# Kernel tuning notes

Hardware: AMD Instinct MI355X
Metric: run time of the kernel (lower is better)

The kernel has to match this reference:

```python
import jax, jax.numpy as jnp
import numpy as np

B, S, D = 2, 2048, 2048
H, KVH = 16, 8
HD = D // H          # 128
REP = H // KVH       # 2
FF = 5504
EPS = 1e-5
THETA = 1e6


def rotate_half(x):
    h = x.shape[-1] // 2
    return jnp.concatenate([-x[..., h:], x[..., :h]], axis=-1)


def rms_norm(x, g):
    v = jnp.mean(x.astype(jnp.float32) ** 2, axis=-1, keepdims=True)
    return (x * jax.lax.rsqrt(v + EPS)).astype(x.dtype) * g


def setup_inputs() -> dict:
    key = jax.random.key(0)
    ks = jax.random.split(key, 10)
    # RoPE tables [S, HD]
    inv_freq = 1.0 / (THETA ** (np.arange(0, HD, 2, dtype=np.float32) / HD))
    t = np.arange(S, dtype=np.float32)
    freqs = np.outer(t, inv_freq)                      # [S, HD/2]
    emb = np.concatenate([freqs, freqs], axis=-1)      # [S, HD]
    sc = 0.02
    return {
        "x": jax.random.normal(ks[0], (B, S, D), jnp.float32),
        "cos": jnp.asarray(np.cos(emb)),
        "sin": jnp.asarray(np.sin(emb)),
        "wq": jax.random.normal(ks[1], (H * HD, D), jnp.float32) * sc,
        "wk": jax.random.normal(ks[2], (KVH * HD, D), jnp.float32) * sc,
        "wv": jax.random.normal(ks[3], (KVH * HD, D), jnp.float32) * sc,
        "wo": jax.random.normal(ks[4], (D, H * HD), jnp.float32) * sc,
        "w_gate": jax.random.normal(ks[5], (FF, D), jnp.float32) * sc,
        "w_up": jax.random.normal(ks[6], (FF, D), jnp.float32) * sc,
        "w_down": jax.random.normal(ks[7], (D, FF), jnp.float32) * sc,
        "g1": jnp.ones((D,), jnp.float32),
        "g2": jnp.ones((D,), jnp.float32),
    }


def reference(x, cos, sin, wq, wk, wv, wo, w_gate, w_up, w_down, g1, g2):
    # ---- attention sub-block ----
    h = rms_norm(x, g1)
    q = (h @ wq.T).reshape(B, S, H, HD)
    k = (h @ wk.T).reshape(B, S, KVH, HD)
    v = (h @ wv.T).reshape(B, S, KVH, HD)
    # RoPE: cos/sin [S,HD] -> broadcast over (B, S, heads, HD) via unsqueeze at head dim
    c = cos[:S][:, None, :]
    s = sin[:S][:, None, :]
    q = q * c + rotate_half(q) * s
    k = k * c + rotate_half(k) * s
    # GQA repeat_kv (repeat_interleave on head dim), then bshd -> bhsd
    k = jnp.repeat(k, REP, axis=2).transpose(0, 2, 1, 3)
    v = jnp.repeat(v, REP, axis=2).transpose(0, 2, 1, 3)
    q = q.transpose(0, 2, 1, 3)
    scores = jnp.einsum("bhqd,bhkd->bhqk", q, k) / jnp.sqrt(jnp.float32(HD))
    causal = jnp.triu(jnp.full((S, S), -jnp.inf, jnp.float32), k=1)
    scores = scores + causal[None, None]
    attn = jax.nn.softmax(scores.astype(jnp.float32), axis=-1).astype(scores.dtype)
    out = jnp.einsum("bhqk,bhkd->bhqd", attn, v)
    out = out.transpose(0, 2, 1, 3).reshape(B, S, H * HD)
    x = x + out @ wo.T
    # ---- SwiGLU MLP sub-block ----
    h2 = rms_norm(x, g2)
    mlp = (jax.nn.silu(h2 @ w_gate.T) * (h2 @ w_up.T)) @ w_down.T
    return x + mlp
```

## Files before the change

kernel.cpp:

```cpp
#include <hip/hip_runtime.h>

#define DM 2048
#define SEQ 2048
#define HD 128
#define FF_ 5504
#define QK_SCALE_L2E 0.12751744f

typedef __bf16 bf16x8 __attribute__((ext_vector_type(8)));
typedef float f32x4 __attribute__((ext_vector_type(4)));
typedef float f32x16 __attribute__((ext_vector_type(16)));
typedef unsigned short u16x8 __attribute__((ext_vector_type(8)));
typedef unsigned int u32x4 __attribute__((ext_vector_type(4)));

typedef __attribute__((address_space(1))) void* gas1;
typedef __attribute__((address_space(3))) void* las3;
#define GLDS16(g, s) __builtin_amdgcn_global_load_lds((gas1)(g), (las3)(s), 16, 0, 0)

static __device__ __forceinline__ float bf2f(unsigned short u) {
  union { unsigned int i; float f; } c; c.i = ((unsigned int)u) << 16; return c.f;
}
static __device__ __forceinline__ unsigned short f2bf(float f) {
  __bf16 b = (__bf16)f;
  return __builtin_bit_cast(unsigned short, b);
}
static __device__ __forceinline__ unsigned int pk2(float a, float b) {
  return (unsigned int)f2bf(a) | ((unsigned int)f2bf(b) << 16);
}
static __device__ __forceinline__ float fexp2(float x) { return exp2f(x); }

__global__ __launch_bounds__(256) void k_convW(const float* __restrict__ wq,
                                               const float* __restrict__ wk,
                                               const float* __restrict__ wv,
                                               const float* __restrict__ wo,
                                               unsigned short* __restrict__ wqkv,
                                               unsigned short* __restrict__ wo_bf) {
  int b = blockIdx.x;
  const float* src;
  unsigned short* dst;
  if (b < 2048)      { src = wq + (size_t)b * DM;            dst = wqkv + (size_t)b * DM; }
  else if (b < 3072) { src = wk + (size_t)(b - 2048) * DM;   dst = wqkv + 4194304 + (size_t)(b - 2048) * DM; }
  else if (b < 4096) { src = wv + (size_t)(b - 3072) * DM;   dst = wqkv + 6291456 + (size_t)(b - 3072) * DM; }
  else               { src = wo + (size_t)(b - 4096) * DM;   dst = wo_bf + (size_t)(b - 4096) * DM; }
  int i = threadIdx.x * 8;
  float4 a = *(const float4*)&src[i];
  float4 c = *(const float4*)&src[i + 4];
  u16x8 o;
  o[0] = f2bf(a.x); o[1] = f2bf(a.y); o[2] = f2bf(a.z); o[3] = f2bf(a.w);
  o[4] = f2bf(c.x); o[5] = f2bf(c.y); o[6] = f2bf(c.z); o[7] = f2bf(c.w);
  *(u16x8*)&dst[i] = o;
}

__global__ __launch_bounds__(256) void k_conv(const float* __restrict__ src,
                                              unsigned short* __restrict__ dst) {
  size_t i = (size_t)(blockIdx.x * 256 + threadIdx.x) * 8;
  float4 a = *(const float4*)&src[i];
  float4 b = *(const float4*)&src[i + 4];
  u16x8 o;
  o[0] = f2bf(a.x); o[1] = f2bf(a.y); o[2] = f2bf(a.z); o[3] = f2bf(a.w);
  o[4] = f2bf(b.x); o[5] = f2bf(b.y); o[6] = f2bf(b.z); o[7] = f2bf(b.w);
  *(u16x8*)&dst[i] = o;
}

__global__ __launch_bounds__(256) void k_conv_gu(const float* __restrict__ g,
                                                 const float* __restrict__ u,
                                                 unsigned short* __restrict__ dst) {
  int i = blockIdx.x * 256 + threadIdx.x;
  int row = i >> 8;
  int c8 = (i & 255) * 8;
  int t = row >> 8, r = row & 255;
  const float* src = (r < 128) ? (g + (size_t)(t * 128 + r) * DM + c8)
                               : (u + (size_t)(t * 128 + (r - 128)) * DM + c8);
  float4 a = *(const float4*)src;
  float4 b = *(const float4*)(src + 4);
  u16x8 o;
  o[0] = f2bf(a.x); o[1] = f2bf(a.y); o[2] = f2bf(a.z); o[3] = f2bf(a.w);
  o[4] = f2bf(b.x); o[5] = f2bf(b.y); o[6] = f2bf(b.z); o[7] = f2bf(b.w);
  *(u16x8*)&dst[(size_t)row * DM + c8] = o;
}

__global__ __launch_bounds__(256) void k_rmsnorm(const float* __restrict__ x,
                                                 const float* __restrict__ g,
                                                 unsigned short* __restrict__ out) {
  int row = blockIdx.x, tid = threadIdx.x;
  const float* xr = x + (size_t)row * DM;
  float4 a = *(const float4*)&xr[tid * 8];
  float4 b = *(const float4*)&xr[tid * 8 + 4];
  float ss = a.x * a.x + a.y * a.y + a.z * a.z + a.w * a.w +
             b.x * b.x + b.y * b.y + b.z * b.z + b.w * b.w;
#pragma unroll
  for (int off = 32; off > 0; off >>= 1) ss += __shfl_xor(ss, off, 64);
  __shared__ float red[4];
  if ((tid & 63) == 0) red[tid >> 6] = ss;
  __syncthreads();
  float rs = rsqrtf((red[0] + red[1] + red[2] + red[3]) * (1.0f / DM) + 1e-5f);
  float4 ga = *(const float4*)&g[tid * 8];
  float4 gb = *(const float4*)&g[tid * 8 + 4];
  u16x8 o;
  o[0] = f2bf(a.x * rs * ga.x); o[1] = f2bf(a.y * rs * ga.y);
  o[2] = f2bf(a.z * rs * ga.z); o[3] = f2bf(a.w * rs * ga.w);
  o[4] = f2bf(b.x * rs * gb.x); o[5] = f2bf(b.y * rs * gb.y);
  o[6] = f2bf(b.z * rs * gb.z); o[7] = f2bf(b.w * rs * gb.w);
  *(u16x8*)&out[(size_t)row * DM + tid * 8] = o;
}

template <int BN, int EPI>
__global__ __launch_bounds__(512, 1) void k_gemm8p(
    const unsigned short* __restrict__ A, const unsigned short* __restrict__ Bt,
    unsigned short* __restrict__ outB, float* __restrict__ outF,
    const float* __restrict__ res, int N, int K,
    const float* __restrict__ cosT, const float* __restrict__ sinT) {
  constexpr int NF = BN / 64;
  constexpr int BUFSZ = (BN == 256) ? 65536 : 49152;
  __shared__ __attribute__((aligned(16))) unsigned char smem[2][BUFSZ];
  const int tid = threadIdx.x, w = tid >> 6, l = tid & 63;
  const int wr = w >> 2, wc = w & 3, lr = l & 15, lg = l >> 4;
  const int bswz = blockIdx.x;
  const int mt = bswz & 15, nt = bswz >> 4;
  const int m0 = mt * 256, n0 = nt * BN;
  const int nkt = K >> 6;

  const int rA0 = tid >> 3;
  const int rB0 = (BN == 256) ? (((tid >> 8) << 6) + ((tid >> 3) & 31)) : (tid >> 3);
  const int sc = ((tid & 7) ^ ((tid >> 3) & 7)) * 8;
  const unsigned short* Abase = A + (size_t)(m0 + rA0) * K + sc;
  const unsigned short* Bbase = Bt + (size_t)(n0 + rB0) * K + sc;

  auto stA = [&](int kt, int h) {
    unsigned char* dst = smem[kt & 1] + h * 16384;
    const unsigned short* s = Abase + (size_t)(h * 64) * K + kt * 64;
    GLDS16(s, dst + tid * 16);
    GLDS16(s + (size_t)128 * K, dst + (512 + tid) * 16);
  };
  auto stB = [&](int kt, int h) {
    unsigned char* dst = smem[kt & 1] + 32768 + h * 16384;
    const unsigned short* s = Bbase + (size_t)(h * 32) * K + kt * 64;
    GLDS16(s, dst + tid * 16);
    GLDS16(s + (size_t)128 * K, dst + (512 + tid) * 16);
  };
  auto stB2 = [&](int kt) {
    unsigned char* dst = smem[kt & 1] + 32768;
    const unsigned short* s = Bbase + kt * 64;
    GLDS16(s, dst + tid * 16);
    GLDS16(s + (size_t)64 * K, dst + (512 + tid) * 16);
  };

  const int aRow = (wr * 64 + lr) * 128;
  const int bRow = (wc * 32 + lr) * 128;
  const int axr = lr & 7;
#define RDA(BUF, M, KK)                                                        \
  (*(const bf16x8*)((BUF) + ((M) >> 2) * 16384 + aRow + ((M) & 3) * 2048 +     \
                    ((((KK) * 4 + lg) ^ axr) << 4)))
#define RDB(BUF, NN, KK)                                                       \
  (*(const bf16x8*)((BUF) + 32768 + ((NN) >> 1) * 16384 + bRow +               \
                    ((NN) & 1) * 2048 + ((((KK) * 4 + lg) ^ axr) << 4)))

  f32x4 acc[8][NF] = {};

  if constexpr (BN == 256) {
    bf16x8 aq[4][2], bq0[2][2], bq1[2][2];
    stA(0, 0); stB(0, 0); stB(0, 1); stA(0, 1);
    stA(1, 0); stB(1, 0); stB(1, 1);
    asm volatile("s_waitcnt vmcnt(6)" ::: "memory");
    __builtin_amdgcn_s_barrier();

#define MMQ(MB, NB, BQ)                                                        \
  _Pragma("unroll") for (int m = 0; m < 4; m++)                                \
    _Pragma("unroll") for (int n = 0; n < 2; n++)                              \
      _Pragma("unroll") for (int kk = 0; kk < 2; kk++)                         \
          acc[(MB) + m][(NB) + n] = __builtin_amdgcn_mfma_f32_16x16x32_bf16(   \
              aq[m][kk], BQ[n][kk], acc[(MB) + m][(NB) + n], 0, 0, 0);

#define KTQ(KT, ST1, ST2, W2V, HASW2, W4V, HASW4)                              \
  {                                                                            \
    const unsigned char* buf = smem[(KT) & 1];                                 \
    _Pragma("unroll") for (int m = 0; m < 4; m++)                              \
      _Pragma("unroll") for (int kk = 0; kk < 2; kk++)                         \
          aq[m][kk] = RDA(buf, m, kk);                                         \
    _Pragma("unroll") for (int n = 0; n < 2; n++)                              \
      _Pragma("unroll") for (int kk = 0; kk < 2; kk++)                         \
          bq0[n][kk] = RDB(buf, n, kk);                                        \
    _Pragma("unroll") for (int n = 0; n < 2; n++)                              \
      _Pragma("unroll") for (int kk = 0; kk < 2; kk++)                         \
          bq1[n][kk] = RDB(buf, n + 2, kk);                                    \
    if (ST1) stA((KT) + 1, 1);                                                 \
    asm volatile("s_waitcnt lgkmcnt(4)" ::: "memory");                         \
    __builtin_amdgcn_sched_barrier(0);                                         \
    __builtin_amdgcn_s_setprio(1);                                             \
    MMQ(0, 0, bq0)                                                             \
    __builtin_amdgcn_s_setprio(0);                                             \
    __builtin_amdgcn_s_barrier();                                              \
    if (ST2) stA((KT) + 2, 0);                                                 \
    asm volatile("s_waitcnt lgkmcnt(0)" ::: "memory");                         \
    __builtin_amdgcn_sched_barrier(0);                                         \
    __builtin_amdgcn_s_setprio(1);                                             \
    MMQ(0, 2, bq1)                                                             \
    __builtin_amdgcn_s_setprio(0);                                             \
    if (HASW2) asm volatile("s_waitcnt vmcnt(%0)" ::"i"(W2V) : "memory");      \
    __builtin_amdgcn_s_barrier();                                              \
    _Pragma("unroll") for (int m = 0; m < 4; m++)                              \
      _Pragma("unroll") for (int kk = 0; kk < 2; kk++)                         \
          aq[m][kk] = RDA(buf, m + 4, kk);                                     \
    if (ST2) stB((KT) + 2, 0);                                                 \
    asm volatile("s_waitcnt lgkmcnt(0)" ::: "memory");                         \
    __builtin_amdgcn_sched_barrier(0);                                         \
    __builtin_amdgcn_s_setprio(1);                                             \
    MMQ(4, 2, bq1)                                                             \
    __builtin_amdgcn_s_setprio(0);                                             \
    __builtin_amdgcn_s_barrier();                                              \
    if (ST2) stB((KT) + 2, 1);                                                 \
    __builtin_amdgcn_s_setprio(1);                                             \
    MMQ(4, 0, bq0)                                                             \
    __builtin_amdgcn_s_setprio(0);                                             \
    if (HASW4) asm volatile("s_waitcnt vmcnt(%0)" ::"i"(W4V) : "memory");      \
    __builtin_amdgcn_s_barrier();                                              \
  }

    for (int kt = 0; kt < nkt - 2; kt++) KTQ(kt, 1, 1, 6, 1, 6, 1);
    KTQ(nkt - 2, 1, 0, 4, 1, 0, 1);
    KTQ(nkt - 1, 0, 0, 0, 0, 0, 0);
#undef KTQ
#undef MMQ
  } else {
    bf16x8 alo[4][2], ahi[4][2], bq[2][2];
    stA(0, 0); stB2(0); stA(0, 1); stA(1, 0); stB2(1);
    asm volatile("s_waitcnt vmcnt(4)" ::: "memory");
    __builtin_amdgcn_s_barrier();

#define MM2(MB, AQ)                                                            \
  _Pragma("unroll") for (int m = 0; m < 4; m++)                                \
    _Pragma("unroll") for (int n = 0; n < 2; n++)                              \
      _Pragma("unroll") for (int kk = 0; kk < 2; kk++)                         \
          acc[(MB) + m][n] = __builtin_amdgcn_mfma_f32_16x16x32_bf16(          \
              AQ[m][kk], bq[n][kk], acc[(MB) + m][n], 0, 0, 0);

#define KT2(KT, ST1, ST2, HASW, WV)                                            \
  {                                                                            \
    const unsigned char* buf = smem[(KT) & 1];                                 \
                     \
    _Pragma("unroll") for (int m = 0; m < 4; m++)                              \
      _Pragma("unroll") for (int kk = 0; kk < 2; kk++)                         \
          alo[m][kk] = RDA(buf, m, kk);                                        \
    _Pragma("unroll") for (int n = 0; n < 2; n++)                              \
      _Pragma("unroll") for (int kk = 0; kk < 2; kk++)                         \
          bq[n][kk] = RDB(buf, n, kk);                                         \
    _Pragma("unroll") for (int m = 0; m < 4; m++)                              \
      _Pragma("unroll") for (int kk = 0; kk < 2; kk++)                         \
          ahi[m][kk] = RDA(buf, m + 4, kk);                                    \
    if (ST1) stA((KT) + 1, 1);                                                 \
    asm volatile("s_waitcnt lgkmcnt(8)" ::: "memory");                         \
    __builtin_amdgcn_sched_barrier(0);                                         \
    __builtin_amdgcn_s_setprio(1);                                             \
    MM2(0, alo)                                                                \
    __builtin_amdgcn_s_setprio(0);                                             \
    __builtin_amdgcn_s_barrier();                                              \
          \
    if (ST2) { stA((KT) + 2, 0); stB2((KT) + 2); }                             \
    asm volatile("s_waitcnt lgkmcnt(0)" ::: "memory");                         \
    __builtin_amdgcn_sched_barrier(0);                                         \
    __builtin_amdgcn_s_setprio(1);                                             \
    MM2(4, ahi)                                                                \
    __builtin_amdgcn_s_setprio(0);                                             \
    if (HASW) asm volatile("s_waitcnt vmcnt(%0)" ::"i"(WV) : "memory");        \
    __builtin_amdgcn_s_barrier();                                              \
  }

    for (int kt = 0; kt < nkt - 2; kt++) KT2(kt, 1, 1, 1, 4);
    KT2(nkt - 2, 1, 0, 1, 0);
    KT2(nkt - 1, 0, 0, 0, 0);
#undef KT2
#undef MM2
  }
#undef RDA
#undef RDB

  const int rbase = wr * 128 + lg * 4;
  const int cbase = wc * (BN / 4) + lr;
  if constexpr (EPI == 0) {
#pragma unroll
    for (int m = 0; m < 8; m++)
#pragma unroll
      for (int n = 0; n < NF; n++)
#pragma unroll
        for (int j = 0; j < 4; j++)
          outB[(size_t)(m0 + rbase + m * 16 + j) * N + n0 + cbase + n * 16] =
              f2bf(acc[m][n][j]);
  } else if constexpr (EPI == 1) {
#pragma unroll
    for (int m = 0; m < 8; m++)
#pragma unroll
      for (int n = 0; n < NF; n++)
#pragma unroll
        for (int j = 0; j < 4; j++) {
          size_t o = (size_t)(m0 + rbase + m * 16 + j) * N + n0 + cbase + n * 16;
          outF[o] = res[o] + acc[m][n][j];
        }
  } else if constexpr (EPI == 2) {
    float* gl = (float*)smem;
    const int ab = n0 >> 1;
    __syncthreads();
#pragma unroll
    for (int half = 0; half < 2; half++) {
      if (wr == half && wc < 2) {
#pragma unroll
        for (int m = 0; m < 8; m++)
#pragma unroll
          for (int n = 0; n < NF; n++)
#pragma unroll
            for (int j = 0; j < 4; j++)
              gl[(m * 16 + lg * 4 + j) * 128 + wc * 64 + n * 16 + lr] = acc[m][n][j];
      }
      __syncthreads();
      if (wr == half && wc >= 2) {
#pragma unroll
        for (int m = 0; m < 8; m++)
#pragma unroll
          for (int n = 0; n < NF; n++)
#pragma unroll
            for (int j = 0; j < 4; j++) {
              int rl = m * 16 + lg * 4 + j;
              int cl = (wc - 2) * 64 + n * 16 + lr;
              float g = gl[rl * 128 + cl];
              float s = g / (1.0f + __expf(-g));
              outB[(size_t)(m0 + half * 128 + rl) * FF_ + ab + cl] = f2bf(s * acc[m][n][j]);
            }
      }
      __syncthreads();
    }
  } else {
    if (nt >= 12) {
#pragma unroll
      for (int m = 0; m < 8; m++)
#pragma unroll
        for (int n = 0; n < NF; n++)
#pragma unroll
          for (int j = 0; j < 4; j++)
            outB[(size_t)(m0 + rbase + m * 16 + j) * N + n0 + cbase + n * 16] =
                f2bf(acc[m][n][j]);
    } else {
      float* gl = (float*)smem;
      const float qs = (nt < 8) ? QK_SCALE_L2E : 1.0f;
      __syncthreads();
      for (int m = 0; m < 8; m++) {
#pragma unroll
        for (int n = 0; n < NF; n++)
#pragma unroll
          for (int j = 0; j < 4; j++)
            gl[wr * 4096 + (lg * 4 + j) * 256 + wc * 64 + n * 16 + lr] = acc[m][n][j];
        __syncthreads();
#pragma unroll
        for (int n = 0; n < NF; n++)
#pragma unroll
          for (int j = 0; j < 4; j++) {
            int c = wc * 64 + n * 16 + lr;
            int d = c & 127;
            int row = m0 + wr * 128 + m * 16 + lg * 4 + j;
            int s = row & (SEQ - 1);
            float own = acc[m][n][j];
            float prt = gl[wr * 4096 + (lg * 4 + j) * 256 + (c ^ 64)];
            float cv = cosT[s * HD + d], sv = sinT[s * HD + d];
            float rot = own * cv + ((d & 64) ? prt : -prt) * sv;
            outB[(size_t)row * N + n0 + c] = f2bf(rot * qs);
          }
        __syncthreads();
      }
    }
  }
}

__global__ __launch_bounds__(256) void k_attn2(const unsigned short* __restrict__ qkv,
                                               unsigned short* __restrict__ out) {
  __shared__ __attribute__((aligned(16))) unsigned short lK[2][64 * 128];
  __shared__ __attribute__((aligned(16))) unsigned short lV[2][128 * 64];
  const float NEG = -3.0e38f;
  int bx = blockIdx.x;
  int qtile = 15 - (bx >> 5);
  int hb = bx & 31;
  int h = hb & 15, b = hb >> 4;
  int q0 = qtile * 128;
  int tid = threadIdx.x, w = tid >> 6, l = tid & 63;
  int l31 = l & 31, half2 = l >> 5;
  const unsigned short* base = qkv + (size_t)b * SEQ * 4096;
  const unsigned short* Kp = base + 2048 + (h >> 1) * HD;
  const unsigned short* Vp = base + 3072 + (h >> 1) * HD;
  const int qw = q0 + w * 32;

  bf16x8 qf[8];
  {
    const unsigned short* qrow = base + (size_t)(qw + l31) * 4096 + h * HD + half2 * 8;
#pragma unroll
    for (int d = 0; d < 8; d++) qf[d] = *(const bf16x8*)(qrow + d * 16);
  }

  f32x16 oacc[4] = {};
  float mrow = NEG, lsum = 0.0f;

  const int vp = tid & 31, vdc = tid >> 5;
  u16x8 va0, va1, vb0, vb1;

  auto stageK = [&](int t) {
    unsigned char* dst = (unsigned char*)lK[t & 1];
#pragma unroll
    for (int i = 0; i < 4; i++) {
      int c = i * 256 + tid;
      int row = c >> 4;
      int g = (c & 15) ^ (row & 7);
      GLDS16(Kp + (size_t)(t * 64 + row) * 4096 + g * 8, dst + (i * 256 + w * 64) * 16);
    }
  };
  auto loadV = [&](int t) {
    const unsigned short* vr = Vp + (size_t)(t * 64 + vp * 2) * 4096 + vdc * 16;
    va0 = *(const u16x8*)(vr);
    va1 = *(const u16x8*)(vr + 8);
    vb0 = *(const u16x8*)(vr + 4096);
    vb1 = *(const u16x8*)(vr + 4096 + 8);
  };

  const int nt = (q0 >> 6) + 2;
  stageK(0);
  loadV(0);

  for (int t = 0; t < nt; t++) {
    __syncthreads();
    {
      unsigned char* lv = (unsigned char*)lV[t & 1];
#pragma unroll
      for (int j = 0; j < 16; j++) {
        int dd = vdc * 16 + j;
        unsigned short lo = (j < 8) ? va0[j] : va1[j - 8];
        unsigned short hi = (j < 8) ? vb0[j] : vb1[j - 8];
        unsigned int pkv = (unsigned int)lo | ((unsigned int)hi << 16);
        *(unsigned int*)(lv + dd * 128 + (((vp >> 2) ^ (dd & 7)) * 16) + (vp & 3) * 4) = pkv;
      }
    }
    __syncthreads();
    if (t + 1 < nt) { stageK(t + 1); loadV(t + 1); }
    const int kv0 = t * 64;
    if (kv0 <= qw + 31) {
      f32x16 sc[2] = {};
      const unsigned char* lk = (const unsigned char*)lK[t & 1];
#pragma unroll
      for (int hh = 0; hh < 2; hh++) {
        int kk = hh * 32 + l31;
        const unsigned char* krow = lk + kk * 256;
#pragma unroll
        for (int d = 0; d < 8; d++) {
          bf16x8 kf = *(const bf16x8*)(krow + (((d * 2 + half2) ^ (kk & 7)) * 16));
          sc[hh] = __builtin_amdgcn_mfma_f32_32x32x16_bf16(kf, qf[d], sc[hh], 0, 0, 0);
        }
      }
      const int qa = qw + l31;
      if (kv0 + 63 > qw) {
#pragma unroll
        for (int hh = 0; hh < 2; hh++)
#pragma unroll
          for (int r = 0; r < 16; r++) {
            int kva = kv0 + hh * 32 + (r & 3) + 8 * (r >> 2) + 4 * half2;
            if (kva > qa) sc[hh][r] = NEG;
          }
      }
      float mx = sc[0][0];
#pragma unroll
      for (int r = 1; r < 16; r++) mx = fmaxf(mx, sc[0][r]);
#pragma unroll
      for (int r = 0; r < 16; r++) mx = fmaxf(mx, sc[1][r]);
      mx = fmaxf(mx, __shfl_xor(mx, 32));
      bool ok = (mx <= mrow + 11.0f);
      if (__ballot(ok) != ~0ull) {
        float mnew = fmaxf(mrow, mx);
        float fct = fexp2(mrow - mnew);
        mrow = mnew;
        lsum *= fct;
#pragma unroll
        for (int r = 0; r < 16; r++) {
          int rr = (r & 3) + 8 * (r >> 2) + 4 * half2;
          float fr = __shfl(fct, rr);
#pragma unroll
          for (int d = 0; d < 4; d++) oacc[d][r] *= fr;
        }
      }
      float ps = 0.0f;
#pragma unroll
      for (int hh = 0; hh < 2; hh++)
#pragma unroll
        for (int r = 0; r < 16; r++) {
          float e = fexp2(sc[hh][r] - mrow);
          sc[hh][r] = e;
          ps += e;
        }
      ps += __shfl_xor(ps, 32);
      lsum += ps;
      const unsigned char* lv = (const unsigned char*)lV[t & 1];
#pragma unroll
      for (int s = 0; s < 4; s++) {
        const int hh = s >> 1;
        const int r0 = (s & 1) * 8;
        unsigned int lo0, lo1, hi0, hi1;
        if (hh == 0) {
          lo0 = pk2(sc[0][r0 + 0], sc[0][r0 + 1]); lo1 = pk2(sc[0][r0 + 2], sc[0][r0 + 3]);
          hi0 = pk2(sc[0][r0 + 4], sc[0][r0 + 5]); hi1 = pk2(sc[0][r0 + 6], sc[0][r0 + 7]);
        } else {
          lo0 = pk2(sc[1][r0 + 0], sc[1][r0 + 1]); lo1 = pk2(sc[1][r0 + 2], sc[1][r0 + 3]);
          hi0 = pk2(sc[1][r0 + 4], sc[1][r0 + 5]); hi1 = pk2(sc[1][r0 + 6], sc[1][r0 + 7]);
        }
        unsigned int s0 = half2 ? lo0 : hi0, s1 = half2 ? lo1 : hi1;
        unsigned int rc0 = (unsigned int)__shfl_xor((int)s0, 32);
        unsigned int rc1 = (unsigned int)__shfl_xor((int)s1, 32);
        u32x4 fr;
        fr[0] = half2 ? rc0 : lo0; fr[1] = half2 ? rc1 : lo1;
        fr[2] = half2 ? hi0 : rc0; fr[3] = half2 ? hi1 : rc1;
        bf16x8 pa = __builtin_bit_cast(bf16x8, fr);
#pragma unroll
        for (int d = 0; d < 4; d++) {
          int dd = d * 32 + l31;
          bf16x8 vf = *(const bf16x8*)(lv + dd * 128 + (((s * 2 + half2) ^ (dd & 7)) * 16));
          oacc[d] = __builtin_amdgcn_mfma_f32_32x32x16_bf16(pa, vf, oacc[d], 0, 0, 0);
        }
      }
    }
  }
  float inv = 1.0f / lsum;
#pragma unroll
  for (int r = 0; r < 16; r++) {
    int rr = (r & 3) + 8 * (r >> 2) + 4 * half2;
    float ir = __shfl(inv, rr);
    size_t ob = ((size_t)(b * SEQ + qw + rr)) * 2048 + h * HD;
#pragma unroll
    for (int d = 0; d < 4; d++)
      out[ob + d * 32 + l31] = f2bf(oacc[d][r] * ir);
  }
}

extern "C" void kernel_launch(void* const* d_in, const int* in_sizes, int n_in,
                              void* d_out, int out_size, void* d_ws, size_t ws_size,
                              hipStream_t stream) {
  const float* x = (const float*)d_in[0];
  const float* cosT = (const float*)d_in[1];
  const float* sinT = (const float*)d_in[2];
  const float* wq = (const float*)d_in[3];
  const float* wk = (const float*)d_in[4];
  const float* wv = (const float*)d_in[5];
  const float* wo = (const float*)d_in[6];
  const float* wg = (const float*)d_in[7];
  const float* wu = (const float*)d_in[8];
  const float* wd = (const float*)d_in[9];
  const float* g1 = (const float*)d_in[10];
  const float* g2 = (const float*)d_in[11];
  float* out = (float*)d_out;
  char* ws = (char*)d_ws;

  unsigned short* wqkv = (unsigned short*)(ws + 0);
  unsigned short* hbuf = (unsigned short*)(ws + 16777216);
  unsigned short* qkv = (unsigned short*)(ws + 33554432);
  unsigned short* attn_o = (unsigned short*)(ws + 67108864);
  unsigned short* wo_bf = (unsigned short*)(ws + 83886080);
  unsigned short* wgu = (unsigned short*)(ws + 33554432);
  unsigned short* act = (unsigned short*)(ws + 92274688);
  unsigned short* wdown = (unsigned short*)(ws + 0);

  k_convW<<<6144, 256, 0, stream>>>(wq, wk, wv, wo, wqkv, wo_bf);
  k_rmsnorm<<<4096, 256, 0, stream>>>(x, g1, hbuf);
  k_gemm8p<256, 3><<<256, 512, 0, stream>>>(hbuf, wqkv, qkv, nullptr, nullptr,
                                            4096, 2048, cosT, sinT);
  k_attn2<<<512, 256, 0, stream>>>(qkv, attn_o);
  k_gemm8p<128, 1><<<256, 512, 0, stream>>>(attn_o, wo_bf, nullptr, out, x,
                                            2048, 2048, nullptr, nullptr);
  k_rmsnorm<<<4096, 256, 0, stream>>>(out, g2, hbuf);
  k_conv_gu<<<11008, 256, 0, stream>>>(wg, wu, wgu);
  k_gemm8p<256, 2><<<688, 512, 0, stream>>>(hbuf, wgu, act, nullptr, nullptr,
                                            11008, 2048, nullptr, nullptr);
  k_conv<<<5504, 256, 0, stream>>>(wd, wdown);
  k_gemm8p<128, 1><<<256, 512, 0, stream>>>(act, wdown, nullptr, out, out,
                                            2048, 5504, nullptr, nullptr);
}
```

Baseline: 565.6 us.

## Merge weight conversion with first RMSNorm, reorder MFMA loops, use max3 reductions

Combines the QKV/O weight conversion and the first RMSNorm into a single launch so one kernel dispatch is saved. The GEMM MFMA loop nests are reordered to put the k-step outermost, changing the issue order of independent accumulator chains. The softmax row-max in attention is rewritten as a chain of three-input max operations to reduce instruction count. Each piece is small; the launch merge saves only one dispatch gap and the loop reorder may shift register pressure.

Measured after the change: 562.1 us, median of 2. No clear change (-0.6%).

```diff
diff --git a/kernel.cpp b/kernel.cpp
--- a/kernel.cpp
+++ b/kernel.cpp
@@ -27,38 +27,56 @@
   return (unsigned int)f2bf(a) | ((unsigned int)f2bf(b) << 16);
 }
 static __device__ __forceinline__ float fexp2(float x) { return exp2f(x); }
-
-__global__ __launch_bounds__(256) void k_convW(const float* __restrict__ wq,
-                                               const float* __restrict__ wk,
-                                               const float* __restrict__ wv,
-                                               const float* __restrict__ wo,
-                                               unsigned short* __restrict__ wqkv,
-                                               unsigned short* __restrict__ wo_bf) {
-  int b = blockIdx.x;
-  const float* src;
-  unsigned short* dst;
-  if (b < 2048)      { src = wq + (size_t)b * DM;            dst = wqkv + (size_t)b * DM; }
-  else if (b < 3072) { src = wk + (size_t)(b - 2048) * DM;   dst = wqkv + 4194304 + (size_t)(b - 2048) * DM; }
-  else if (b < 4096) { src = wv + (size_t)(b - 3072) * DM;   dst = wqkv + 6291456 + (size_t)(b - 3072) * DM; }
-  else               { src = wo + (size_t)(b - 4096) * DM;   dst = wo_bf + (size_t)(b - 4096) * DM; }
-  int i = threadIdx.x * 8;
-  float4 a = *(const float4*)&src[i];
-  float4 c = *(const float4*)&src[i + 4];
-  u16x8 o;
-  o[0] = f2bf(a.x); o[1] = f2bf(a.y); o[2] = f2bf(a.z); o[3] = f2bf(a.w);
-  o[4] = f2bf(c.x); o[5] = f2bf(c.y); o[6] = f2bf(c.z); o[7] = f2bf(c.w);
-  *(u16x8*)&dst[i] = o;
-}
-
-__global__ __launch_bounds__(256) void k_conv(const float* __restrict__ src,
-                                              unsigned short* __restrict__ dst) {
-  size_t i = (size_t)(blockIdx.x * 256 + threadIdx.x) * 8;
-  float4 a = *(const float4*)&src[i];
-  float4 b = *(const float4*)&src[i + 4];
-  u16x8 o;
-  o[0] = f2bf(a.x); o[1] = f2bf(a.y); o[2] = f2bf(a.z); o[3] = f2bf(a.w);
-  o[4] = f2bf(b.x); o[5] = f2bf(b.y); o[6] = f2bf(b.z); o[7] = f2bf(b.w);
-  *(u16x8*)&dst[i] = o;
+static __device__ __forceinline__ float max3f(float a, float b, float c) {
+  return fmaxf(fmaxf(a, b), c);
+}
+
+__global__ __launch_bounds__(256) void k_prep(const float* __restrict__ wq,
+                                              const float* __restrict__ wk,
+                                              const float* __restrict__ wv,
+                                              const float* __restrict__ wo,
+                                              unsigned short* __restrict__ wqkv,
+                                              unsigned short* __restrict__ wo_bf,
+                                              const float* __restrict__ x,
+                                              const float* __restrict__ g1,
+                                              unsigned short* __restrict__ hbuf) {
+  int b = blockIdx.x, tid = threadIdx.x;
+  if (b < 6144) {
+    const float* src;
+    unsigned short* dst;
+    if (b < 2048)      { src = wq + (size_t)b * DM;          dst = wqkv + (size_t)b * DM; }
+    else if (b < 3072) { src = wk + (size_t)(b - 2048) * DM; dst = wqkv + 4194304 + (size_t)(b - 2048) * DM; }
+    else if (b < 4096) { src = wv + (size_t)(b - 3072) * DM; dst = wqkv + 6291456 + (size_t)(b - 3072) * DM; }
+    else               { src = wo + (size_t)(b - 4096) * DM; dst = wo_bf + (size_t)(b - 4096) * DM; }
+    int i = tid * 8;
+    float4 a = *(const float4*)&src[i];
+    float4 c = *(const float4*)&src[i + 4];
+    u16x8 o;
+    o[0] = f2bf(a.x); o[1] = f2bf(a.y); o[2] = f2bf(a.z); o[3] = f2bf(a.w);
+    o[4] = f2bf(c.x); o[5] = f2bf(c.y); o[6] = f2bf(c.z); o[7] = f2bf(c.w);
+    *(u16x8*)&dst[i] = o;
+  } else {
+    int row = b - 6144;
+    const float* xr = x + (size_t)row * DM;
+    float4 a = *(const float4*)&xr[tid * 8];
+    float4 c = *(const float4*)&xr[tid * 8 + 4];
+    float ss = a.x * a.x + a.y * a.y + a.z * a.z + a.w * a.w +
+               c.x * c.x + c.y * c.y + c.z * c.z + c.w * c.w;
+#pragma unroll
+    for (int off = 32; off > 0; off >>= 1) ss += __shfl_xor(ss, off, 64);
+    __shared__ float red[4];
+    if ((tid & 63) == 0) red[tid >> 6] = ss;
+    __syncthreads();
+    float rs = rsqrtf((red[0] + red[1] + red[2] + red[3]) * (1.0f / DM) + 1e-5f);
+    float4 ga = *(const float4*)&g1[tid * 8];
+    float4 gb = *(const float4*)&g1[tid * 8 + 4];
+    u16x8 o;
+    o[0] = f2bf(a.x * rs * ga.x); o[1] = f2bf(a.y * rs * ga.y);
+    o[2] = f2bf(a.z * rs * ga.z); o[3] = f2bf(a.w * rs * ga.w);
+    o[4] = f2bf(c.x * rs * gb.x); o[5] = f2bf(c.y * rs * gb.y);
+    o[6] = f2bf(c.z * rs * gb.z); o[7] = f2bf(c.w * rs * gb.w);
+    *(u16x8*)&hbuf[(size_t)row * DM + tid * 8] = o;
+  }
 }
 
 __global__ __launch_bounds__(256) void k_conv_gu(const float* __restrict__ g,
@@ -76,6 +94,17 @@
   o[0] = f2bf(a.x); o[1] = f2bf(a.y); o[2] = f2bf(a.z); o[3] = f2bf(a.w);
   o[4] = f2bf(b.x); o[5] = f2bf(b.y); o[6] = f2bf(b.z); o[7] = f2bf(b.w);
   *(u16x8*)&dst[(size_t)row * DM + c8] = o;
+}
+
+__global__ __launch_bounds__(256) void k_conv(const float* __restrict__ src,
+                                              unsigned short* __restrict__ dst) {
+  size_t i = (size_t)(blockIdx.x * 256 + threadIdx.x) * 8;
+  float4 a = *(const float4*)&src[i];
+  float4 b = *(const float4*)&src[i + 4];
+  u16x8 o;
+  o[0] = f2bf(a.x); o[1] = f2bf(a.y); o[2] = f2bf(a.z); o[3] = f2bf(a.w);
+  o[4] = f2bf(b.x); o[5] = f2bf(b.y); o[6] = f2bf(b.z); o[7] = f2bf(b.w);
+  *(u16x8*)&dst[i] = o;
 }
 
 __global__ __launch_bounds__(256) void k_rmsnorm(const float* __restrict__ x,
@@ -164,9 +193,9 @@
     __builtin_amdgcn_s_barrier();
 
 #define MMQ(MB, NB, BQ)                                                        \
-  _Pragma("unroll") for (int m = 0; m < 4; m++)                                \
-    _Pragma("unroll") for (int n = 0; n < 2; n++)                              \
-      _Pragma("unroll") for (int kk = 0; kk < 2; kk++)                         \
+  _Pragma("unroll") for (int kk = 0; kk < 2; kk++)                             \
+    _Pragma("unroll") for (int m = 0; m < 4; m++)                              \
+      _Pragma("unroll") for (int n = 0; n < 2; n++)                            \
           acc[(MB) + m][(NB) + n] = __builtin_amdgcn_mfma_f32_16x16x32_bf16(   \
               aq[m][kk], BQ[n][kk], acc[(MB) + m][(NB) + n], 0, 0, 0);
 
@@ -227,16 +256,15 @@
     __builtin_amdgcn_s_barrier();
 
 #define MM2(MB, AQ)                                                            \
-  _Pragma("unroll") for (int m = 0; m < 4; m++)                                \
-    _Pragma("unroll") for (int n = 0; n < 2; n++)                              \
-      _Pragma("unroll") for (int kk = 0; kk < 2; kk++)                         \
+  _Pragma("unroll") for (int kk = 0; kk < 2; kk++)                             \
+    _Pragma("unroll") for (int m = 0; m < 4; m++)                              \
+      _Pragma("unroll") for (int n = 0; n < 2; n++)                            \
           acc[(MB) + m][n] = __builtin_amdgcn_mfma_f32_16x16x32_bf16(          \
               AQ[m][kk], bq[n][kk], acc[(MB) + m][n], 0, 0, 0);
 
 #define KT2(KT, ST1, ST2, HASW, WV)                                            \
   {                                                                            \
     const unsigned char* buf = smem[(KT) & 1];                                 \
-                     \
     _Pragma("unroll") for (int m = 0; m < 4; m++)                              \
       _Pragma("unroll") for (int kk = 0; kk < 2; kk++)                         \
           alo[m][kk] = RDA(buf, m, kk);                                        \
@@ -253,7 +281,6 @@
     MM2(0, alo)                                                                \
     __builtin_amdgcn_s_setprio(0);                                             \
     __builtin_amdgcn_s_barrier();                                              \
-          \
     if (ST2) { stA((KT) + 2, 0); stB2((KT) + 2); }                             \
     asm volatile("s_waitcnt lgkmcnt(0)" ::: "memory");                         \
     __builtin_amdgcn_sched_barrier(0);                                         \
@@ -458,11 +485,23 @@
             if (kva > qa) sc[hh][r] = NEG;
           }
       }
-      float mx = sc[0][0];
-#pragma unroll
-      for (int r = 1; r < 16; r++) mx = fmaxf(mx, sc[0][r]);
-#pragma unroll
-      for (int r = 0; r < 16; r++) mx = fmaxf(mx, sc[1][r]);
+      float m0v = fmaxf(sc[0][0], sc[0][1]);
+      m0v = max3f(m0v, sc[0][2], sc[0][3]);
+      m0v = max3f(m0v, sc[0][4], sc[0][5]);
+      m0v = max3f(m0v, sc[0][6], sc[0][7]);
+      m0v = max3f(m0v, sc[0][8], sc[0][9]);
+      m0v = max3f(m0v, sc[0][10], sc[0][11]);
+      m0v = max3f(m0v, sc[0][12], sc[0][13]);
+      m0v = max3f(m0v, sc[0][14], sc[0][15]);
+      float m1v = fmaxf(sc[1][0], sc[1][1]);
+      m1v = max3f(m1v, sc[1][2], sc[1][3]);
+      m1v = max3f(m1v, sc[1][4], sc[1][5]);
+      m1v = max3f(m1v, sc[1][6], sc[1][7]);
+      m1v = max3f(m1v, sc[1][8], sc[1][9]);
+      m1v = max3f(m1v, sc[1][10], sc[1][11]);
+      m1v = max3f(m1v, sc[1][12], sc[1][13]);
+      m1v = max3f(m1v, sc[1][14], sc[1][15]);
+      float mx = fmaxf(m0v, m1v);
       mx = fmaxf(mx, __shfl_xor(mx, 32));
       bool ok = (mx <= mrow + 11.0f);
       if (__ballot(ok) != ~0ull) {
@@ -557,8 +596,7 @@
   unsigned short* act = (unsigned short*)(ws + 92274688);
   unsigned short* wdown = (unsigned short*)(ws + 0);
 
-  k_convW<<<6144, 256, 0, stream>>>(wq, wk, wv, wo, wqkv, wo_bf);
-  k_rmsnorm<<<4096, 256, 0, stream>>>(x, g1, hbuf);
+  k_prep<<<10240, 256, 0, stream>>>(wq, wk, wv, wo, wqkv, wo_bf, x, g1, hbuf);
   k_gemm8p<256, 3><<<256, 512, 0, stream>>>(hbuf, wqkv, qkv, nullptr, nullptr,
                                             4096, 2048, cosT, sinT);
   k_attn2<<<512, 256, 0, stream>>>(qkv, attn_o);
```
